# Performance work log

Measured on AMD Instinct MI355X. Metric: run time of the kernel, lower is better.

The kernel has to match this reference:

```python
import jax, jax.numpy as jnp
import numpy as np

# --- model constants (reconstructed LIF + exponential-PSP semantics) ---
V_TH = 1.0        # spike threshold
V_DECAY = 0.9     # membrane leak per ms
PSP_DECAY = 0.8   # postsynaptic-potential filter decay
BETA = 5.0        # surrogate-gradient sharpness
D = 16            # spike_buffer depth (max synaptic delay)
H = W = 64
T = 200
N = H * W
N_DEL = 11        # number of delayed synapses


def setup_inputs() -> dict:
    key = jax.random.key(0)
    ks = jax.random.split(key, 5)
    stim = jax.random.uniform(ks[0], (H, W, T), dtype=jnp.float32) * 8.0
    scale = 1.0 / np.sqrt(N)
    W_sa_in = jax.random.normal(ks[1], (N, N), dtype=jnp.float32) * scale
    W_ra_in = jax.random.normal(ks[2], (N, N), dtype=jnp.float32) * scale
    W_del = jax.random.normal(ks[3], (N_DEL, N, N), dtype=jnp.float32) * scale
    delays = jax.random.randint(ks[4], (N_DEL, N), 0, D, dtype=jnp.int32)
    return {"stim": stim, "W_sa_in": W_sa_in, "W_ra_in": W_ra_in,
            "W_del": W_del, "delays": delays}


def _spike(v):
    """Hard threshold forward, sigmoid surrogate gradient (straight-through)."""
    hard = (v >= V_TH).astype(v.dtype)
    soft = jax.nn.sigmoid(BETA * (v - V_TH))
    return soft + jax.lax.stop_gradient(hard - soft)


def reference(stim, W_sa_in, W_ra_in, W_del, delays):
    n = stim.shape[0] * stim.shape[1]
    t_len = stim.shape[2]
    # stimulus preprocessing (feedforward):
    sa_stim = (stim - 3.0).reshape(n, t_len)                    # [N, T]
    d = jnp.abs(jnp.diff(stim, axis=2)) * 10.0                  # [H, W, T-1]
    d = d.at[:, :, :3].set(0.0)
    ra_stim = jnp.concatenate(
        [jnp.zeros(stim.shape[:2] + (1,), stim.dtype), d], axis=2
    ).reshape(n, t_len)                                         # [N, T]

    idx = jnp.arange(n)
    read_col = D - 1 - delays                                   # [11, N] constant gather columns

    def lif(v, buf, li, inp):
        vn = v[li] * V_DECAY + inp
        s = _spike(vn)
        vn = vn * (1.0 - s)                                     # reset on spike
        v = v.at[li].set(vn)
        buf = buf.at[li].set(
            jnp.concatenate([buf[li][:, 1:], s[:, None]], axis=1))  # roll, newest last
        return v, buf, s

    def syn(psp, k, buf_pre):
        dsp = buf_pre[idx, read_col[k]]                         # per-pre delayed spikes [N]
        p = psp[k] * PSP_DECAY + W_del[k] @ dsp
        return psp.at[k].set(p), p

    def step(carry, xs):
        v, buf, psp = carry
        sa_x, ra_x = xs
        # SA pathway (layers 0,1,2 <-> state rows 0,1,2)
        v, buf, s0 = lif(v, buf, 0, W_sa_in @ sa_x)
        psp, i1 = syn(psp, 0, buf[0])
        v, buf, s1 = lif(v, buf, 1, i1)
        psp, pn1 = syn(psp, 1, buf[0])
        psp, pn2 = syn(psp, 2, buf[1])
        v, buf, s2 = lif(v, buf, 2, 2.0 * pn1 - pn2)
        # RA pathway (state rows 3,4,5)
        v, buf, s3 = lif(v, buf, 3, W_ra_in @ ra_x)
        psp, j1 = syn(psp, 3, buf[3])
        v, buf, s4 = lif(v, buf, 4, j1)
        psp, qn1 = syn(psp, 4, buf[3])
        psp, qn2 = syn(psp, 5, buf[4])
        v, buf, s5 = lif(v, buf, 5, 2.0 * qn1 - qn2)
        # CN (state rows 6 = IN, 7 = PN)
        psp, cin_sa = syn(psp, 6, buf[2])
        psp, cin_ra = syn(psp, 8, buf[5])
        v, buf, s6 = lif(v, buf, 6, cin_sa + cin_ra)
        psp, cpn_sa = syn(psp, 7, buf[2])
        psp, cpn_ra = syn(psp, 9, buf[5])
        psp, inh = syn(psp, 10, buf[6])
        v, buf, s7 = lif(v, buf, 7, 2.0 * cpn_sa + 2.0 * cpn_ra - inh)
        return (v, buf, psp), jnp.stack([s0, s1, s2, s3, s4, s5, s6, s7])

    carry0 = (jnp.zeros((8, n), stim.dtype),
              jnp.zeros((8, n, D), stim.dtype),
              jnp.zeros((N_DEL, n), stim.dtype))
    xs = (sa_stim[:, 1:].T, ra_stim[:, 1:].T)                   # [T-1, N] each
    _, spikes = jax.lax.scan(step, carry0, xs)                  # [T-1, 8, N]
    return jnp.transpose(spikes, (1, 2, 0))                     # [8, N, T-1]
```

## Files before the change

### kernel.cpp

```cpp
#include <hip/hip_runtime.h>

#define NN   4096
#define TLEN 200
#define NT   199
#define NW   8
#define NTP  256
#define TN   ((size_t)NT * NN)
#define TN2  ((size_t)NN * NTP)

#define BM 128
#define BT 128
#define BK 32
#define BMP 132
#define BTP 132

typedef __attribute__((ext_vector_type(8))) short short8;
typedef __attribute__((ext_vector_type(16))) float f32x16;


__global__ void xmat(const int* __restrict__ delays, const unsigned* __restrict__ Sb,
                     unsigned short* __restrict__ Xg, int kpack, int prepack) {
  const int ki = blockIdx.y;
  const int k = (kpack >> (4 * ki)) & 15;
  const int pre = (prepack >> (4 * ki)) & 15;
  const int jb = blockIdx.x * 32;
  __shared__ unsigned Xw[32][8];
  const int tid = threadIdx.x;
  {
    const int jj = tid >> 3, tw = tid & 7;
    const int j = jb + jj;
    const int d = delays[(size_t)k * NN + j];
    const int tsrc = tw * 32 - d;
    const int w0 = tsrc >> 5, sh = tsrc & 31;
    const unsigned lo = (w0 >= 0 && w0 < NW) ? Sb[(size_t)pre * NW * NN + (size_t)w0 * NN + j] : 0u;
    const unsigned hi = (w0 + 1 >= 0 && w0 + 1 < NW) ? Sb[(size_t)pre * NW * NN + (size_t)(w0 + 1) * NN + j] : 0u;
    Xw[jj][tw] = sh ? ((lo >> sh) | (hi << (32 - sh))) : lo;
  }
  __syncthreads();
  {
    const int t = tid;
    const int tw = t >> 5, tb = t & 31;
    unsigned out[16];
    #pragma unroll
    for (int q = 0; q < 16; ++q) {
      const unsigned b0 = (Xw[2 * q][tw] >> tb) & 1u;
      const unsigned b1 = (Xw[2 * q + 1][tw] >> tb) & 1u;
      out[q] = (b0 ? 0x3F80u : 0u) | (b1 ? 0x3F800000u : 0u);
    }
    unsigned short* dst = Xg + ((size_t)k * NTP + t) * NN + jb;
    #pragma unroll
    for (int q = 0; q < 4; ++q) *(uint4*)(dst + 8 * q) = *(uint4*)&out[4 * q];
  }
}

__global__ __launch_bounds__(256, 2) void gsyn(const float* __restrict__ Wdel,
    const unsigned short* __restrict__ Xg, float* __restrict__ u,
    int Slog, int kpack, int slotpack) {
  const int z = blockIdx.y;
  const int ki = z >> Slog, s = z & ((1 << Slog) - 1);
  const int k = (kpack >> (4 * ki)) & 15;
  const int slot = ((slotpack >> (6 * ki)) & 63) + s;
  const int NJ = NN >> Slog;
  const int jbase = s * NJ;
  const float* __restrict__ Wk = Wdel + (size_t)k * NN * NN;
  const unsigned short* __restrict__ Xk = Xg + (size_t)k * NTP * NN;
  float* __restrict__ uo = u + (size_t)slot * TN2;

  __shared__ __align__(16) unsigned char smem[3 * 8192];

  const int i0 = blockIdx.x * 128;
  const int tid = threadIdx.x;
  const int wave = tid >> 6, lane = tid & 63;
  const int m = lane & 31, hb = lane >> 5;
  const int wi = wave >> 1, wt = wave & 1;

  f32x16 acc[2][4];
  #pragma unroll
  for (int a = 0; a < 2; ++a)
    #pragma unroll
    for (int b = 0; b < 4; ++b) acc[a][b] = 0.0f;

  const int rb = tid >> 3, kc = tid & 7;
  const unsigned short* __restrict__ xp0 = Xk + (size_t)(wt * 128 + m) * NN + jbase;

  for (int j0 = 0; j0 < NJ; j0 += 32) {
    short8 xb[2][4];
    #pragma unroll
    for (int h2 = 0; h2 < 2; ++h2)
      #pragma unroll
      for (int b = 0; b < 4; ++b)
        xb[h2][b] = *(const short8*)(xp0 + (size_t)(b * 32) * NN + j0 + h2 * 16 + hb * 8);

    #pragma unroll
    for (int mm = 0; mm < 4; ++mm) {
      const int r = rb + 32 * mm;
      const float4 w4 = *(const float4*)&Wk[(size_t)(i0 + r) * NN + jbase + j0 + kc * 4];
      unsigned h[4], md[4], lo[4];
      const float wv[4] = {w4.x, w4.y, w4.z, w4.w};
      #pragma unroll
      for (int e = 0; e < 4; ++e) {
        const unsigned ub = __float_as_uint(wv[e]);
        h[e] = ub >> 16;
        const float r1 = wv[e] - __uint_as_float(ub & 0xFFFF0000u);
        const unsigned u1 = __float_as_uint(r1);
        md[e] = u1 >> 16;
        const float r2 = r1 - __uint_as_float(u1 & 0xFFFF0000u);
        lo[e] = __float_as_uint(r2) >> 16;
      }
      const unsigned base = (unsigned)((r * 64 + kc * 8) ^ ((r & 7) << 4));
      uint2 p0; p0.x = (h[1] << 16) | h[0];  p0.y = (h[3] << 16) | h[2];
      uint2 p1; p1.x = (md[1] << 16) | md[0]; p1.y = (md[3] << 16) | md[2];
      uint2 p2; p2.x = (lo[1] << 16) | lo[0]; p2.y = (lo[3] << 16) | lo[2];
      *(uint2*)(smem + base)          = p0;
      *(uint2*)(smem + 8192 + base)   = p1;
      *(uint2*)(smem + 16384 + base)  = p2;
    }
    __syncthreads();
    #pragma unroll
    for (int h2 = 0; h2 < 2; ++h2) {
      const int cb = h2 * 32 + hb * 16;
      #pragma unroll
      for (int a = 0; a < 2; ++a) {
        const int ra = wi * 64 + a * 32 + m;
        const unsigned abase = (unsigned)((ra * 64 + cb) ^ ((ra & 7) << 4));
        const short8 a0 = *(const short8*)(smem + abase);
        const short8 a1 = *(const short8*)(smem + 8192 + abase);
        const short8 a2 = *(const short8*)(smem + 16384 + abase);
        #pragma unroll
        for (int b = 0; b < 4; ++b) {
          acc[a][b] = __builtin_amdgcn_mfma_f32_32x32x16_bf16(a0, xb[h2][b], acc[a][b], 0, 0, 0);
          acc[a][b] = __builtin_amdgcn_mfma_f32_32x32x16_bf16(a1, xb[h2][b], acc[a][b], 0, 0, 0);
          acc[a][b] = __builtin_amdgcn_mfma_f32_32x32x16_bf16(a2, xb[h2][b], acc[a][b], 0, 0, 0);
        }
      }
    }
    __syncthreads();
  }
  #pragma unroll
  for (int a = 0; a < 2; ++a)
    #pragma unroll
    for (int b = 0; b < 4; ++b) {
      const int tt2 = wt * 128 + b * 32 + m;
      #pragma unroll
      for (int r = 0; r < 16; ++r) {
        const int ii = i0 + wi * 64 + a * 32 + (r & 3) + 8 * (r >> 2) + 4 * hb;
        uo[(size_t)ii * NTP + tt2] = acc[a][b][r];
      }
    }
}

__global__ __launch_bounds__(256, 2) void gstim(const float* __restrict__ Wsa,
    const float* __restrict__ Wra, const float* __restrict__ stim,
    float* __restrict__ u) {
  const int zi = blockIdx.z;
  const int mode = zi >> 2, s = zi & 3;
  const int slot = 64 + 4 * mode + s;
  const int NJ = NN >> 2;
  const int jbase = s * NJ;
  const float* __restrict__ W = mode ? Wra : Wsa;
  float* __restrict__ uo = u + (size_t)slot * TN2;

  __shared__ float Ws[BK][BMP];
  __shared__ float Xs[BK][BTP];
  const int i0 = blockIdx.x * BM;
  const int t0 = blockIdx.y * BT;
  const int tid = threadIdx.x;
  const int rg = tid >> 4, cg = tid & 15;
  float acc[8][8] = {};

  for (int k0 = 0; k0 < NJ; k0 += BK) {
    {
      const int kk4 = tid & 7, r = tid >> 3;
      const int sw = 4 * kk4;
      #pragma unroll
      for (int mq = 0; mq < 4; ++mq) {
        const int rr = r + 32 * mq;
        const float4 w = *(const float4*)&W[(size_t)(i0 + rr) * NN + jbase + k0 + 4 * kk4];
        const int pc = rr ^ sw;
        Ws[4 * kk4 + 0][pc] = w.x; Ws[4 * kk4 + 1][pc] = w.y;
        Ws[4 * kk4 + 2][pc] = w.z; Ws[4 * kk4 + 3][pc] = w.w;
      }
    }
    {
      const int kk = tid >> 3, sb8 = tid & 7;
      const int j = jbase + k0 + kk;
      #pragma unroll
      for (int q = 0; q < 4; ++q) {
        float4 xv;
        float* xp = (float*)&xv;
        #pragma unroll
        for (int e = 0; e < 4; ++e) {
          const int tt = t0 + 16 * sb8 + 4 * q + e;
          float x = 0.0f;
          if (tt < NT) {
            const int tc = tt + 1;
            if (mode == 0) {
              x = stim[(size_t)j * TLEN + tc] - 3.0f;
            } else {
              x = (tc >= 4)
                ? fabsf(stim[(size_t)j * TLEN + tc] - stim[(size_t)j * TLEN + tc - 1]) * 10.0f
                : 0.0f;
            }
          }
          xp[e] = x;
        }
        *(float4*)&Xs[kk][16 * sb8 + 4 * q] = xv;
      }
    }
    __syncthreads();
    #pragma unroll
    for (int kk = 0; kk < BK; ++kk) {
      const int wsw = 4 * (kk >> 2);
      const float4 ra = *(const float4*)&Ws[kk][(rg * 4) ^ wsw];
      const float4 rbv = *(const float4*)&Ws[kk][(64 + rg * 4) ^ wsw];
      const float4 ca = *(const float4*)&Xs[kk][cg * 4];
      const float4 cb = *(const float4*)&Xs[kk][64 + cg * 4];
      const float rv[8] = {ra.x, ra.y, ra.z, ra.w, rbv.x, rbv.y, rbv.z, rbv.w};
      const float cv[8] = {ca.x, ca.y, ca.z, ca.w, cb.x, cb.y, cb.z, cb.w};
      #pragma unroll
      for (int a = 0; a < 8; ++a)
        #pragma unroll
        for (int b = 0; b < 8; ++b) acc[a][b] += rv[a] * cv[b];
    }
    __syncthreads();
  }
  #pragma unroll
  for (int a = 0; a < 8; ++a) {
    const int ia = i0 + ((a < 4) ? (rg * 4 + a) : (64 + rg * 4 + (a - 4)));
    #pragma unroll
    for (int bh = 0; bh < 2; ++bh) {
      float4 o;
      o.x = acc[a][bh * 4 + 0]; o.y = acc[a][bh * 4 + 1];
      o.z = acc[a][bh * 4 + 2]; o.w = acc[a][bh * 4 + 3];
      *(float4*)&uo[(size_t)ia * NTP + t0 + bh * 64 + cg * 4] = o;
    }
  }
}

template<int S>
__device__ __forceinline__ float4 sumS4(const float* __restrict__ u, int slot, int tg, int j) {
  float4 r = {0.f, 0.f, 0.f, 0.f};
  #pragma unroll
  for (int q = 0; q < S; ++q) {
    const float4 a = *(const float4*)&u[(size_t)(slot + q) * TN2 + (size_t)j * NTP + tg];
    r.x += a.x; r.y += a.y; r.z += a.z; r.w += a.w;
  }
  return r;
}
__device__ __forceinline__ float fidx(const float4& v, int q) {
  return q == 0 ? v.x : q == 1 ? v.y : q == 2 ? v.z : v.w;
}

__device__ __forceinline__ void flush_bits(unsigned* sb, int j, int t, unsigned& bits) {
  if ((t & 31) == 31 || t == NT - 1) { sb[(size_t)(t >> 5) * NN + j] = bits; bits = 0; }
}

__global__ void scan_a(const float* __restrict__ u, unsigned* __restrict__ Sb) {
  const int j = blockIdx.x * 64 + threadIdx.x;
  const int base = 64 + 4 * blockIdx.y;
  unsigned* sb = Sb + (size_t)(blockIdx.y ? 3 : 0) * NW * NN;
  float v = 0.f; unsigned bits = 0;
  for (int tg = 0; tg < NT; tg += 4) {
    const float4 in4 = sumS4<4>(u, base, tg, j);
    #pragma unroll
    for (int q = 0; q < 4; ++q) {
      const int t = tg + q;
      if (t < NT) {
        float vn = v * 0.9f + fidx(in4, q);
        unsigned s = vn >= 1.0f;
        v = s ? 0.f : vn;
        bits |= s << (t & 31);
        flush_bits(sb, j, t, bits);
      }
    }
  }
}

__global__ void scan_b(const float* __restrict__ u, unsigned* __restrict__ Sb,
                       float* __restrict__ p1s, float* __restrict__ p4s) {
  const int j = blockIdx.x * 64 + threadIdx.x;
  const int sa = blockIdx.y;
  const int baseA = sa ? 8 : 0, baseB = sa ? 12 : 4;
  float* ps = sa ? p4s : p1s;
  unsigned* sb = Sb + (size_t)(sa ? 4 : 1) * NW * NN;
  float v = 0.f, pa = 0.f, pb = 0.f; unsigned bits = 0;
  for (int tg = 0; tg < NT; tg += 4) {
    const float4 A4 = sumS4<4>(u, baseA, tg, j);
    const float4 B4 = sumS4<4>(u, baseB, tg, j);
    #pragma unroll
    for (int q = 0; q < 4; ++q) {
      const int t = tg + q;
      if (t < NT) {
        pa = pa * 0.8f + fidx(A4, q);
        float vn = v * 0.9f + pa;
        unsigned s = vn >= 1.0f;
        v = s ? 0.f : vn;
        bits |= s << (t & 31);
        flush_bits(sb, j, t, bits);
        pb = pb * 0.8f + fidx(B4, q);
        ps[(size_t)t * NN + j] = 2.0f * pb;
      }
    }
  }
}

__global__ void scan_c(const float* __restrict__ u, unsigned* __restrict__ Sb,
                       const float* __restrict__ p1s, const float* __restrict__ p4s) {
  const int j = blockIdx.x * 64 + threadIdx.x;
  const int sa = blockIdx.y;
  const int base = sa ? 24 : 16;
  const float* ps = sa ? p4s : p1s;
  unsigned* sb = Sb + (size_t)(sa ? 5 : 2) * NW * NN;
  float v = 0.f, p = 0.f; unsigned bits = 0;
  for (int tg = 0; tg < NT; tg += 4) {
    const float4 A4 = sumS4<8>(u, base, tg, j);
    float P[4];
    #pragma unroll
    for (int q = 0; q < 4; ++q)
      P[q] = (tg + q < NT) ? ps[(size_t)(tg + q) * NN + j] : 0.0f;
    #pragma unroll
    for (int q = 0; q < 4; ++q) {
      const int t = tg + q;
      if (t < NT) {
        p = p * 0.8f + fidx(A4, q);
        float vn = v * 0.9f + (P[q] - p);
        unsigned s = vn >= 1.0f;
        v = s ? 0.f : vn;
        bits |= s << (t & 31);
        flush_bits(sb, j, t, bits);
      }
    }
  }
}

__global__ void scan_d(const float* __restrict__ u, unsigned* __restrict__ Sb,
                       float* __restrict__ p79s) {
  const int j = blockIdx.x * 64 + threadIdx.x;
  if (blockIdx.y == 0) {
    unsigned* sb = Sb + (size_t)6 * NW * NN;
    float v = 0.f, p6 = 0.f, p8 = 0.f; unsigned bits = 0;
    for (int tg = 0; tg < NT; tg += 4) {
      const float4 A4 = sumS4<4>(u, 32, tg, j);
      const float4 B4 = sumS4<4>(u, 40, tg, j);
      #pragma unroll
      for (int q = 0; q < 4; ++q) {
        const int t = tg + q;
        if (t < NT) {
          p6 = p6 * 0.8f + fidx(A4, q);
          p8 = p8 * 0.8f + fidx(B4, q);
          float vn = v * 0.9f + (p6 + p8);
          unsigned s = vn >= 1.0f;
          v = s ? 0.f : vn;
          bits |= s << (t & 31);
          flush_bits(sb, j, t, bits);
        }
      }
    }
  } else {
    float p7 = 0.f, p9 = 0.f;
    for (int tg = 0; tg < NT; tg += 4) {
      const float4 A4 = sumS4<4>(u, 36, tg, j);
      const float4 B4 = sumS4<4>(u, 44, tg, j);
      #pragma unroll
      for (int q = 0; q < 4; ++q) {
        const int t = tg + q;
        if (t < NT) {
          p7 = p7 * 0.8f + fidx(A4, q);
          p9 = p9 * 0.8f + fidx(B4, q);
          p79s[(size_t)t * NN + j] = 2.0f * p7 + 2.0f * p9;
        }
      }
    }
  }
}

__global__ void scan_e(const float* __restrict__ u, unsigned* __restrict__ Sb,
                       const float* __restrict__ p79s) {
  const int j = blockIdx.x * 64 + threadIdx.x;
  unsigned* sb = Sb + (size_t)7 * NW * NN;
  float v = 0.f, p = 0.f; unsigned bits = 0;
  for (int tg = 0; tg < NT; tg += 4) {
    const float4 A4 = sumS4<16>(u, 48, tg, j);
    float P[4];
    #pragma unroll
    for (int q = 0; q < 4; ++q)
      P[q] = (tg + q < NT) ? p79s[(size_t)(tg + q) * NN + j] : 0.0f;
    #pragma unroll
    for (int q = 0; q < 4; ++q) {
      const int t = tg + q;
      if (t < NT) {
        p = p * 0.8f + fidx(A4, q);
        float vn = v * 0.9f + (P[q] - p);
        unsigned s = vn >= 1.0f;
        v = s ? 0.f : vn;
        bits |= s << (t & 31);
        flush_bits(sb, j, t, bits);
      }
    }
  }
}

__global__ void expand_k(const unsigned* __restrict__ Sb, float* __restrict__ out) {
  const int j = blockIdx.x * 256 + threadIdx.x;
  const int w = blockIdx.y, li = blockIdx.z;
  unsigned bits = Sb[((size_t)li * NW + w) * NN + j];
  float* o = out + ((size_t)li * NN + j) * NT + w * 32;
  int nb = NT - w * 32; if (nb > 32) nb = 32;
  for (int b = 0; b < nb; ++b) o[b] = (float)((bits >> b) & 1u);
}

extern "C" void kernel_launch(void* const* d_in, const int* in_sizes, int n_in,
                              void* d_out, int out_size, void* d_ws, size_t ws_size,
                              hipStream_t stream) {
  const float* stim   = (const float*)d_in[0];
  const float* Wsa    = (const float*)d_in[1];
  const float* Wra    = (const float*)d_in[2];
  const float* Wdel   = (const float*)d_in[3];
  const int*   delays = (const int*)d_in[4];
  float* out = (float*)d_out;
  float* ws  = (float*)d_ws;

  float* u    = ws;
  float* p1s  = u + 72 * TN2;
  float* p4s  = p1s + TN;
  float* p79s = p4s + TN;
  unsigned* Sb = (unsigned*)(p79s + TN);
  unsigned short* Xg = (unsigned short*)(Sb + (size_t)8 * NW * NN);
  size_t need = (72 * TN2 + 3 * TN + (size_t)8 * NW * NN) * 4 + (size_t)11 * NTP * NN * 2;
  if (ws_size < need) return;

  hipMemsetAsync(Sb, 0, (size_t)8 * NW * NN * sizeof(unsigned), stream);

  const dim3 gmf(NN / 128, 16);
  gstim<<<dim3(NN / BM, 2, 8), 256, 0, stream>>>(Wsa, Wra, stim, u);
  scan_a<<<dim3(64, 2), 64, 0, stream>>>(u, Sb);

  xmat<<<dim3(NN / 32, 4), 256, 0, stream>>>(delays, Sb, Xg, 0x4310, 0x3300);
  gsyn<<<gmf, 256, 0, stream>>>(Wdel, Xg, u, 2, 0x4310,
                                0 | (4 << 6) | (8 << 12) | (12 << 18));
  scan_b<<<dim3(64, 2), 64, 0, stream>>>(u, Sb, p1s, p4s);

  xmat<<<dim3(NN / 32, 2), 256, 0, stream>>>(delays, Sb, Xg, 0x52, 0x41);
  gsyn<<<gmf, 256, 0, stream>>>(Wdel, Xg, u, 3, 0x52, 16 | (24 << 6));
  scan_c<<<dim3(64, 2), 64, 0, stream>>>(u, Sb, p1s, p4s);

  xmat<<<dim3(NN / 32, 4), 256, 0, stream>>>(delays, Sb, Xg, 0x9876, 0x5522);
  gsyn<<<gmf, 256, 0, stream>>>(Wdel, Xg, u, 2, 0x9876,
                                32 | (36 << 6) | (40 << 12) | (44 << 18));
  scan_d<<<dim3(64, 2), 64, 0, stream>>>(u, Sb, p79s);

  xmat<<<dim3(NN / 32, 1), 256, 0, stream>>>(delays, Sb, Xg, 10, 6);
  gsyn<<<gmf, 256, 0, stream>>>(Wdel, Xg, u, 4, 10, 48);
  scan_e<<<dim3(64, 1), 64, 0, stream>>>(u, Sb, p79s);

  expand_k<<<dim3(16, 7, 8), 256, 0, stream>>>(Sb, out);
}
```

Measured before the change: 831.1 us.

## Stage spike matrix tile through LDS and skip padded time columns in gsyn

The gsyn kernel now loads the bf16 spike (X) tile cooperatively into swizzled shared memory once per K-step, and each wave reads its B fragments from LDS, replacing the per-wave direct global loads that fetched overlapping data. It also skips the last 32-column time block (t >= 224) for the second wave half, since only 199 of the 256 padded time steps are real, which removes a quarter of that half's MFMAs and stores. The cost is 16 KB more LDS per block, which may reduce occupancy under the launch bound of 2, plus an extra LDS write and read pass.

```diff
diff --git a/kernel.cpp b/kernel.cpp
--- a/kernel.cpp
+++ b/kernel.cpp
@@ -66,13 +66,15 @@
   const unsigned short* __restrict__ Xk = Xg + (size_t)k * NTP * NN;
   float* __restrict__ uo = u + (size_t)slot * TN2;
 
-  __shared__ __align__(16) unsigned char smem[3 * 8192];
+  __shared__ __align__(16) unsigned char smem[3 * 8192 + 16384];
+  #define XOFF 24576
 
   const int i0 = blockIdx.x * 128;
   const int tid = threadIdx.x;
   const int wave = tid >> 6, lane = tid & 63;
   const int m = lane & 31, hb = lane >> 5;
   const int wi = wave >> 1, wt = wave & 1;
+  const int bmax = wt ? 3 : 4;
 
   f32x16 acc[2][4];
   #pragma unroll
@@ -81,16 +83,9 @@
     for (int b = 0; b < 4; ++b) acc[a][b] = 0.0f;
 
   const int rb = tid >> 3, kc = tid & 7;
-  const unsigned short* __restrict__ xp0 = Xk + (size_t)(wt * 128 + m) * NN + jbase;
+  const unsigned short* __restrict__ xsrc = Xk + (size_t)tid * NN + jbase;
 
   for (int j0 = 0; j0 < NJ; j0 += 32) {
-    short8 xb[2][4];
-    #pragma unroll
-    for (int h2 = 0; h2 < 2; ++h2)
-      #pragma unroll
-      for (int b = 0; b < 4; ++b)
-        xb[h2][b] = *(const short8*)(xp0 + (size_t)(b * 32) * NN + j0 + h2 * 16 + hb * 8);
-
     #pragma unroll
     for (int mm = 0; mm < 4; ++mm) {
       const int r = rb + 32 * mm;
@@ -115,10 +110,26 @@
       *(uint2*)(smem + 8192 + base)   = p1;
       *(uint2*)(smem + 16384 + base)  = p2;
     }
+    {
+      const int t = tid;
+      #pragma unroll
+      for (int q = 0; q < 4; ++q) {
+        const uint4 xv = *(const uint4*)(xsrc + j0 + q * 8);
+        *(uint4*)(smem + XOFF + ((t * 64 + q * 16) ^ ((t & 7) << 4))) = xv;
+      }
+    }
     __syncthreads();
     #pragma unroll
     for (int h2 = 0; h2 < 2; ++h2) {
       const int cb = h2 * 32 + hb * 16;
+      short8 bfr[4];
+      #pragma unroll
+      for (int b = 0; b < 4; ++b) {
+        if (b < bmax) {
+          const int tr = wt * 128 + b * 32 + m;
+          bfr[b] = *(const short8*)(smem + XOFF + ((tr * 64 + cb) ^ ((tr & 7) << 4)));
+        }
+      }
       #pragma unroll
       for (int a = 0; a < 2; ++a) {
         const int ra = wi * 64 + a * 32 + m;
@@ -128,9 +139,11 @@
         const short8 a2 = *(const short8*)(smem + 16384 + abase);
         #pragma unroll
         for (int b = 0; b < 4; ++b) {
-          acc[a][b] = __builtin_amdgcn_mfma_f32_32x32x16_bf16(a0, xb[h2][b], acc[a][b], 0, 0, 0);
-          acc[a][b] = __builtin_amdgcn_mfma_f32_32x32x16_bf16(a1, xb[h2][b], acc[a][b], 0, 0, 0);
-          acc[a][b] = __builtin_amdgcn_mfma_f32_32x32x16_bf16(a2, xb[h2][b], acc[a][b], 0, 0, 0);
+          if (b < bmax) {
+            acc[a][b] = __builtin_amdgcn_mfma_f32_32x32x16_bf16(a0, bfr[b], acc[a][b], 0, 0, 0);
+            acc[a][b] = __builtin_amdgcn_mfma_f32_32x32x16_bf16(a1, bfr[b], acc[a][b], 0, 0, 0);
+            acc[a][b] = __builtin_amdgcn_mfma_f32_32x32x16_bf16(a2, bfr[b], acc[a][b], 0, 0, 0);
+          }
         }
       }
     }
@@ -140,13 +153,16 @@
   for (int a = 0; a < 2; ++a)
     #pragma unroll
     for (int b = 0; b < 4; ++b) {
-      const int tt2 = wt * 128 + b * 32 + m;
-      #pragma unroll
-      for (int r = 0; r < 16; ++r) {
-        const int ii = i0 + wi * 64 + a * 32 + (r & 3) + 8 * (r >> 2) + 4 * hb;
-        uo[(size_t)ii * NTP + tt2] = acc[a][b][r];
-      }
-    }
+      if (b < bmax) {
+        const int tt2 = wt * 128 + b * 32 + m;
+        #pragma unroll
+        for (int r = 0; r < 16; ++r) {
+          const int ii = i0 + wi * 64 + a * 32 + (r & 3) + 8 * (r >> 2) + 4 * hb;
+          uo[(size_t)ii * NTP + tt2] = acc[a][b][r];
+        }
+      }
+    }
+  #undef XOFF
 }
 
 __global__ __launch_bounds__(256, 2) void gstim(const float* __restrict__ Wsa,
```

After: 821.0 us. No clear change (-1.2%).
